# Optimization experiments

Measured on AMD Instinct MI355X. Metric: run time of the kernel, lower is better.

The kernel has to match this reference:

```python
import jax, jax.numpy as jnp
from jax import lax
import numpy as np

NUM_HEAD = 12
EPS = 1e-5            # torch LayerNorm default
NEG_INF = 1.0e12      # self.inf_value in the source
LEAKY_SLOPE = 0.01    # torch LeakyReLU default
MASK_FIRST = True     # maskedAtten=True applies only to block 0


def _layer_norm(x, s, b):
    m = jnp.mean(x, axis=-1, keepdims=True)
    v = jnp.var(x, axis=-1, keepdims=True)
    return (x - m) / jnp.sqrt(v + EPS) * s + b


def _forward(x, conv_w, conv_b, pos, ln0_s, ln0_b, Wq, bq, Wk, bk, Wv, bv,
             Wo, bo, ln1_s, ln1_b, W1, b1, W2, b2, proj_w, proj_b):
    B, C, H, W = x.shape
    E = conv_w.shape[0]
    P = conv_w.shape[-1]
    hd = E // NUM_HEAD

    # patch embed: Conv2d(C, E, P, stride=P)
    h = lax.conv_general_dilated(x, conv_w, (P, P), 'VALID',
                                 dimension_numbers=('NCHW', 'OIHW', 'NCHW'))
    h = h + conv_b[None, :, None, None]
    L = h.shape[2] * h.shape[3]
    h = h.reshape(B, E, L).transpose(0, 2, 1) + pos  # (B, L, E)

    causal = jnp.triu(jnp.ones((L, L), dtype=bool), 1)
    n_layers = Wq.shape[0]
    for i in range(n_layers):
        # --- attention block ---
        xn = _layer_norm(h, ln0_s[i], ln0_b[i])
        q = (xn @ Wq[i] + bq[i]).reshape(B, L, NUM_HEAD, hd).transpose(0, 2, 1, 3)
        k = (xn @ Wk[i] + bk[i]).reshape(B, L, NUM_HEAD, hd).transpose(0, 2, 1, 3)
        v = (xn @ Wv[i] + bv[i]).reshape(B, L, NUM_HEAD, hd).transpose(0, 2, 1, 3)
        scores = jnp.einsum('bhqd,bhkd->bhqk', q, k) * (hd ** -0.5)
        if i == 0 and MASK_FIRST:
            scores = jnp.where(causal, -NEG_INF, scores)
        a = jax.nn.softmax(scores, axis=-1)
        o = jnp.einsum('bhqk,bhkd->bhqd', a, v)  # (B, NH, L, hd)
        # faithful to torch source: reshape(bs, l, emb) WITHOUT permuting heads back
        o = o.reshape(B, L, E)
        o = o @ Wo[i] + bo[i]
        h = o + h  # residual onto pre-LN input
        # --- MLP block ---
        xr = _layer_norm(h, ln1_s[i], ln1_b[i])
        m = xr @ W1[i] + b1[i]
        m = jnp.where(m >= 0, m, LEAKY_SLOPE * m)
        m = m @ W2[i] + b2[i]
        h = m + xr  # residual onto post-LN (as in source)

    y = h @ proj_w + proj_b               # (B, L, C*P*P)
    y = y.transpose(0, 2, 1).reshape(B, C, H, W)
    return y


def setup_inputs() -> dict:
    key = jax.random.key(0)
    B, C, H, W = 8, 3, 384, 384
    P, E, NL = 16, 768, 8
    FF = 4 * E
    L = (H // P) * (W // P)  # 576
    CPP = C * P * P          # 768
    s = 0.02
    ks = jax.random.split(key, 24)
    f32 = jnp.float32
    inp = {
        'x': jax.random.normal(ks[0], (B, C, H, W), f32),
        'conv_w': jax.random.normal(ks[1], (E, C, P, P), f32) * s,
        'conv_b': jax.random.normal(ks[2], (E,), f32) * s,
        'pos': jax.random.normal(ks[3], (1, L, E), f32),
        'ln0_s': jnp.ones((NL, E), f32),
        'ln0_b': jnp.zeros((NL, E), f32),
        'Wq': jax.random.normal(ks[4], (NL, E, E), f32) * s,
        'bq': jax.random.normal(ks[5], (NL, E), f32) * s,
        'Wk': jax.random.normal(ks[6], (NL, E, E), f32) * s,
        'bk': jax.random.normal(ks[7], (NL, E), f32) * s,
        'Wv': jax.random.normal(ks[8], (NL, E, E), f32) * s,
        'bv': jax.random.normal(ks[9], (NL, E), f32) * s,
        'Wo': jax.random.normal(ks[10], (NL, E, E), f32) * s,
        'bo': jax.random.normal(ks[11], (NL, E), f32) * s,
        'ln1_s': jnp.ones((NL, E), f32),
        'ln1_b': jnp.zeros((NL, E), f32),
        'W1': jax.random.normal(ks[12], (NL, E, FF), f32) * s,
        'b1': jax.random.normal(ks[13], (NL, FF), f32) * s,
        'W2': jax.random.normal(ks[14], (NL, FF, E), f32) * s,
        'b2': jax.random.normal(ks[15], (NL, E), f32) * s,
        'proj_w': jax.random.normal(ks[16], (E, CPP), f32) * s,
        'proj_b': jax.random.normal(ks[17], (CPP,), f32) * s,
    }
    return inp


def reference(x, conv_w, conv_b, pos, ln0_s, ln0_b, Wq, bq, Wk, bk, Wv, bv,
              Wo, bo, ln1_s, ln1_b, W1, b1, W2, b2, proj_w, proj_b):
    return _forward(x, conv_w, conv_b, pos, ln0_s, ln0_b, Wq, bq, Wk, bk,
                    Wv, bv, Wo, bo, ln1_s, ln1_b, W1, b1, W2, b2,
                    proj_w, proj_b)
```

## Files before the change

kernel.cpp:

```cpp
#include <hip/hip_runtime.h>
#include <hip/hip_bf16.h>
#include <stdint.h>

#define NLAYERS 8
#define LSEQ 576
#define EMB 768
#define NHEAD 12
#define HDIM 64
#define FFDIM 3072
#define BLROWS 4608

typedef __attribute__((ext_vector_type(8))) short short8;
typedef __attribute__((ext_vector_type(4))) float floatx4;

__device__ __forceinline__ float b2f(short s) {
    union { float f; uint32_t u; } x; x.u = ((uint32_t)(uint16_t)s) << 16; return x.f;
}
__device__ __forceinline__ short f2b(float f) {
    union { float f; uint32_t u; } x; x.f = f;
    uint32_t r = x.u + 0x7fffu + ((x.u >> 16) & 1u);
    return (short)(r >> 16);
}

#define GLDS16(gp, lp) __builtin_amdgcn_global_load_lds( \
    (const __attribute__((address_space(1))) void*)(gp), \
    (__attribute__((address_space(3))) void*)(lp), 16, 0, 0)

__device__ __forceinline__ void xcd_remap(int& bx, int& by) {
    const int gx = gridDim.x;
    const int n  = gx * gridDim.y;
    const int orig = by * gx + bx;
    const int q = n >> 3, r = n & 7;
    const int xcd = orig & 7;
    const int wgid = (xcd < r ? xcd * (q + 1) : r * (q + 1) + (xcd - r) * q) + (orig >> 3);
    bx = wgid % gx;
    by = wgid / gx;
}

template<bool ADD_POS, bool RES_F32, bool LEAKY, bool OUT_F32>
__global__ __launch_bounds__(256)
void gemm_bt(const short* __restrict__ A, const short* __restrict__ Bt,
             const float* __restrict__ bias, const float* __restrict__ pos,
             const float* __restrict__ resf, void* __restrict__ Cout,
             int N, int K)
{
    __shared__ short As[2 * 64 * 64];
    __shared__ short Bs[2 * 128 * 64];
    int bx = blockIdx.x, by = blockIdx.y;
    xcd_remap(bx, by);
    const int t    = threadIdx.x;
    const int lane = t & 63;
    const int w    = t >> 6;
    const int m0   = by * 64;
    const int n0   = bx * 128;
    const int wm   = (w >> 1) * 32;
    const int wn   = (w & 1) * 64;

    floatx4 acc[2][4];
#pragma unroll
    for (int i = 0; i < 2; ++i)
#pragma unroll
        for (int j = 0; j < 4; ++j)
            acc[i][j] = (floatx4){0.f, 0.f, 0.f, 0.f};

    const int srow = t >> 3;
    const int sch  = t & 7;

    const short* Ag = A  + (size_t)m0 * K;
    const short* Bg = Bt + (size_t)n0 * K;

#define STAGE(buf, k0)                                                              \
    {                                                                               \
        _Pragma("unroll")                                                           \
        for (int i = 0; i < 2; ++i) {                                               \
            int row = srow + i * 32;                                                \
            GLDS16(Ag + (size_t)row * K + (k0) + ((sch ^ (row & 7)) << 3),          \
                   &As[(buf) * 4096 + (size_t)(t + i * 256) * 8]);                  \
        }                                                                           \
        _Pragma("unroll")                                                           \
        for (int i = 0; i < 4; ++i) {                                               \
            int row = srow + i * 32;                                                \
            GLDS16(Bg + (size_t)row * K + (k0) + ((sch ^ (row & 7)) << 3),          \
                   &Bs[(buf) * 8192 + (size_t)(t + i * 256) * 8]);                  \
        }                                                                           \
    }

    STAGE(0, 0);
    __syncthreads();
    int cur = 0;
    for (int k0 = 0; k0 < K; k0 += 64) {
        if (k0 + 64 < K) STAGE(cur ^ 1, k0 + 64);
#pragma unroll
        for (int ks = 0; ks < 2; ++ks) {
            short8 af[2], bf[4];
#pragma unroll
            for (int i = 0; i < 2; ++i) {
                int row = wm + i * 16 + (lane & 15);
                int ch  = (ks * 4 + (lane >> 4)) ^ (row & 7);
                af[i] = *(const short8*)&As[cur * 4096 + row * 64 + ch * 8];
            }
#pragma unroll
            for (int j = 0; j < 4; ++j) {
                int row = wn + j * 16 + (lane & 15);
                int ch  = (ks * 4 + (lane >> 4)) ^ (row & 7);
                bf[j] = *(const short8*)&Bs[cur * 8192 + row * 64 + ch * 8];
            }
#pragma unroll
            for (int i = 0; i < 2; ++i)
#pragma unroll
                for (int j = 0; j < 4; ++j)
                    acc[i][j] = __builtin_amdgcn_mfma_f32_16x16x32_bf16(af[i], bf[j], acc[i][j], 0, 0, 0);
        }
        __syncthreads();
        cur ^= 1;
    }
#undef STAGE

    const int colb = n0 + wn + (lane & 15);
    const int rowb = m0 + wm + ((lane >> 4) * 4);
#pragma unroll
    for (int i = 0; i < 2; ++i) {
#pragma unroll
        for (int j = 0; j < 4; ++j) {
            const int col = colb + j * 16;
            const float bv = bias[col];
#pragma unroll
            for (int r = 0; r < 4; ++r) {
                const int row = rowb + i * 16 + r;
                float v = acc[i][j][r] + bv;
                if constexpr (ADD_POS) v += pos[(size_t)(row % LSEQ) * N + col];
                if constexpr (RES_F32) v += resf[(size_t)row * N + col];
                if constexpr (LEAKY)   v = v >= 0.f ? v : 0.01f * v;
                if constexpr (OUT_F32) ((float*)Cout)[(size_t)row * N + col] = v;
                else                   ((short*)Cout)[(size_t)row * N + col] = f2b(v);
            }
        }
    }
}

__global__ __launch_bounds__(256)
void ln_kernel(const float* __restrict__ h, const float* __restrict__ g,
               const float* __restrict__ bbias, short* __restrict__ outb,
               float* __restrict__ outf)
{
    const int row = blockIdx.x;
    const float* x = h + (size_t)row * EMB;
    const int t = threadIdx.x;
    float v0 = x[t], v1 = x[t + 256], v2 = x[t + 512];
    float s  = v0 + v1 + v2;
    float ss = v0 * v0 + v1 * v1 + v2 * v2;
#pragma unroll
    for (int m = 1; m < 64; m <<= 1) {
        s  += __shfl_xor(s, m, 64);
        ss += __shfl_xor(ss, m, 64);
    }
    __shared__ float red[8];
    if ((t & 63) == 0) { red[t >> 6] = s; red[4 + (t >> 6)] = ss; }
    __syncthreads();
    float S  = red[0] + red[1] + red[2] + red[3];
    float SS = red[4] + red[5] + red[6] + red[7];
    float mean = S * (1.f / 768.f);
    float var  = SS * (1.f / 768.f) - mean * mean;
    float rstd = rsqrtf(var + 1e-5f);
    const size_t base = (size_t)row * EMB;
#pragma unroll
    for (int q = 0; q < 3; ++q) {
        int e = t + q * 256;
        float v = (q == 0 ? v0 : (q == 1 ? v1 : v2));
        float y = (v - mean) * rstd * g[e] + bbias[e];
        outb[base + e] = f2b(y);
        if (outf) outf[base + e] = y;
    }
}

__global__ __launch_bounds__(256)
void repack_kv(const short* __restrict__ qkv, short* __restrict__ kp, short* __restrict__ vt)
{
    const int kt = blockIdx.x, bh = blockIdx.y;
    const int b = bh / 12, h = bh % 12;
    const int t = threadIdx.x;
#pragma unroll
    for (int i = 0; i < 2; ++i) {
        int flat = i * 256 + t;
        int key = flat >> 3, c = flat & 7;
        short8 vK = *(const short8*)(qkv + ((size_t)(b * LSEQ) + kt * 64 + key) * 2304 + 768 + h * 64 + c * 8);
        *(short8*)(kp + ((size_t)bh * LSEQ + kt * 64 + key) * 64 + 8 * (c ^ (key & 7))) = vK;
    }
    __shared__ short tile[64][65];
    const int tx = t & 63, ty = t >> 6;
#pragma unroll
    for (int r = 0; r < 16; ++r) {
        int k = ty * 16 + r;
        tile[k][tx] = qkv[((size_t)(b * LSEQ) + kt * 64 + k) * 2304 + 1536 + h * 64 + tx];
    }
    __syncthreads();
#pragma unroll
    for (int r = 0; r < 16; ++r) {
        int d = ty * 16 + r;
        vt[((size_t)bh * 64 + d) * LSEQ + kt * 64 + (tx ^ ((d & 7) << 3))] = tile[tx][d];
    }
}

__global__ __launch_bounds__(256)
void attn_mfma(const short* __restrict__ qkv, const short* __restrict__ kp,
               const short* __restrict__ vt, short* __restrict__ oout, int causal)
{
    const int qt = blockIdx.x, bh = blockIdx.y;
    const int b = bh / 12, h = bh % 12;
    const int t = threadIdx.x, lane = t & 63, w = t >> 6;

    __shared__ short Ks[64 * 64];
    __shared__ short Vs[64 * 64];
    __shared__ short Plds[4][16][72];

    const int nrow = lane & 15;
    const int kch  = (lane >> 4) * 8;
    const int swz  = (lane & 7) << 3;

    short8 aq[2];
    {
        const short* qrow = qkv + ((size_t)(b * LSEQ) + qt * 64 + w * 16 + nrow) * 2304 + h * 64 + kch;
        aq[0] = *(const short8*)qrow;
        aq[1] = *(const short8*)(qrow + 32);
    }

    float m[4], lsum[4];
    floatx4 oacc[4];
#pragma unroll
    for (int r = 0; r < 4; ++r) { m[r] = -3e38f; lsum[r] = 0.f; }
#pragma unroll
    for (int j = 0; j < 4; ++j) oacc[j] = (floatx4){0.f, 0.f, 0.f, 0.f};

    const int ktend = causal ? qt : 8;
    const short* ksrc = kp + ((size_t)bh * LSEQ) * 64;
    const short* vsrc = vt + ((size_t)bh * 64) * LSEQ;

    for (int kt = 0; kt <= ktend; ++kt) {
        __syncthreads();
        {
            const short* kt_src = ksrc + (size_t)(kt * 64) * 64;
            GLDS16(kt_src + (size_t)t * 8,          &Ks[(size_t)t * 8]);
            GLDS16(kt_src + (size_t)(t + 256) * 8,  &Ks[(size_t)(t + 256) * 8]);
            int f0 = t, f1 = t + 256;
            GLDS16(vsrc + (size_t)(f0 >> 3) * LSEQ + kt * 64 + (f0 & 7) * 8, &Vs[(size_t)f0 * 8]);
            GLDS16(vsrc + (size_t)(f1 >> 3) * LSEQ + kt * 64 + (f1 & 7) * 8, &Vs[(size_t)f1 * 8]);
        }
        __syncthreads();

        floatx4 sc[4];
#pragma unroll
        for (int j = 0; j < 4; ++j) sc[j] = (floatx4){0.f, 0.f, 0.f, 0.f};
#pragma unroll
        for (int s = 0; s < 2; ++s) {
#pragma unroll
            for (int j = 0; j < 4; ++j) {
                short8 bk = *(const short8*)&Ks[(16 * j + nrow) * 64 + ((kch + 32 * s) ^ swz)];
                sc[j] = __builtin_amdgcn_mfma_f32_16x16x32_bf16(aq[s], bk, sc[j], 0, 0, 0);
            }
        }
        float sv[4][4];
#pragma unroll
        for (int j = 0; j < 4; ++j)
#pragma unroll
            for (int r = 0; r < 4; ++r) {
                float v = sc[j][r] * 0.125f;
                if (causal && kt == qt) {
                    int key = kt * 64 + 16 * j + nrow;
                    int qr  = qt * 64 + w * 16 + (lane >> 4) * 4 + r;
                    if (key > qr) v = -1e12f;
                }
                sv[j][r] = v;
            }
#pragma unroll
        for (int r = 0; r < 4; ++r) {
            float tm = fmaxf(fmaxf(sv[0][r], sv[1][r]), fmaxf(sv[2][r], sv[3][r]));
            tm = fmaxf(tm, __shfl_xor(tm, 1, 64));
            tm = fmaxf(tm, __shfl_xor(tm, 2, 64));
            tm = fmaxf(tm, __shfl_xor(tm, 4, 64));
            tm = fmaxf(tm, __shfl_xor(tm, 8, 64));
            float nm = fmaxf(m[r], tm);
            float c  = __expf(m[r] - nm);
            m[r] = nm;
            float ps = 0.f;
#pragma unroll
            for (int j = 0; j < 4; ++j) {
                float p = __expf(sv[j][r] - nm);
                sv[j][r] = p;
                ps += p;
            }
            lsum[r] = lsum[r] * c + ps;
#pragma unroll
            for (int j = 0; j < 4; ++j) oacc[j][r] *= c;
        }
#pragma unroll
        for (int j = 0; j < 4; ++j)
#pragma unroll
            for (int r = 0; r < 4; ++r)
                Plds[w][(lane >> 4) * 4 + r][16 * j + nrow] = f2b(sv[j][r]);
        short8 ap[2];
#pragma unroll
        for (int s = 0; s < 2; ++s)
            ap[s] = *(const short8*)&Plds[w][nrow][kch + 32 * s];
#pragma unroll
        for (int s = 0; s < 2; ++s) {
#pragma unroll
            for (int j = 0; j < 4; ++j) {
                short8 bv = *(const short8*)&Vs[(16 * j + nrow) * 64 + ((kch + 32 * s) ^ swz)];
                oacc[j] = __builtin_amdgcn_mfma_f32_16x16x32_bf16(ap[s], bv, oacc[j], 0, 0, 0);
            }
        }
    }

    float inv[4];
#pragma unroll
    for (int r = 0; r < 4; ++r) {
        float L = lsum[r];
        L += __shfl_xor(L, 1, 64);
        L += __shfl_xor(L, 2, 64);
        L += __shfl_xor(L, 4, 64);
        L += __shfl_xor(L, 8, 64);
        inv[r] = 1.f / L;
    }
#pragma unroll
    for (int j = 0; j < 4; ++j)
#pragma unroll
        for (int r = 0; r < 4; ++r) {
            size_t lq = (size_t)qt * 64 + w * 16 + (lane >> 4) * 4 + r;
            oout[((size_t)bh * LSEQ + lq) * 64 + 16 * j + nrow] = f2b(oacc[j][r] * inv[r]);
        }
}

__global__ void transpose_f2b(const float* __restrict__ in, short* __restrict__ out,
                              int R, int C, long long ibs, long long obs)
{
    __shared__ float tile[32][33];
    const int b = blockIdx.z;
    const float* inb = in + (long long)b * ibs;
    short* outb = out + (long long)b * obs;
    const int r0 = blockIdx.y * 32, c0 = blockIdx.x * 32;
    const int tx = threadIdx.x, ty = threadIdx.y;
#pragma unroll
    for (int i = 0; i < 32; i += 8) tile[ty + i][tx] = inb[(size_t)(r0 + ty + i) * C + c0 + tx];
    __syncthreads();
#pragma unroll
    for (int i = 0; i < 32; i += 8) outb[(size_t)(c0 + ty + i) * R + r0 + tx] = f2b(tile[tx][ty + i]);
}

__global__ void transpose_f2f(const float* __restrict__ in, float* __restrict__ out,
                              int R, int C, long long ibs, long long obs)
{
    __shared__ float tile[32][33];
    const int b = blockIdx.z;
    const float* inb = in + (long long)b * ibs;
    float* outb = out + (long long)b * obs;
    const int r0 = blockIdx.y * 32, c0 = blockIdx.x * 32;
    const int tx = threadIdx.x, ty = threadIdx.y;
#pragma unroll
    for (int i = 0; i < 32; i += 8) tile[ty + i][tx] = inb[(size_t)(r0 + ty + i) * C + c0 + tx];
    __syncthreads();
#pragma unroll
    for (int i = 0; i < 32; i += 8) outb[(size_t)(c0 + ty + i) * R + r0 + tx] = tile[tx][ty + i];
}

__global__ void concat_qkv_bias(const float* __restrict__ bq, const float* __restrict__ bk,
                                const float* __restrict__ bv, float* __restrict__ out)
{
    int i = blockIdx.x * 256 + threadIdx.x;
    int layer = i / 2304, j = i % 2304;
    float v;
    if (j < 768)       v = bq[layer * 768 + j];
    else if (j < 1536) v = bk[layer * 768 + j - 768];
    else               v = bv[layer * 768 + j - 1536];
    out[i] = v;
}

__global__ void im2col_kernel(const float* __restrict__ x, short* __restrict__ xcol)
{
    const size_t idx = (size_t)blockIdx.x * 256 + threadIdx.x;
    const int k = (int)(idx % 768);
    const size_t m = idx / 768;
    const int c  = k >> 8;
    const int ky = (k >> 4) & 15;
    const int kx = k & 15;
    const int b  = (int)(m / 576);
    const int l  = (int)(m % 576);
    const int ph = l / 24, pw = l % 24;
    xcol[idx] = f2b(x[((size_t)(b * 3 + c) * 384 + ph * 16 + ky) * 384 + pw * 16 + kx]);
}

__global__ void cast_f32_b16(const float* __restrict__ in, short* __restrict__ out, int n)
{
    int i = blockIdx.x * 256 + threadIdx.x;
    if (i < n) out[i] = f2b(in[i]);
}

extern "C" void kernel_launch(void* const* d_in, const int* in_sizes, int n_in,
                              void* d_out, int out_size, void* d_ws, size_t ws_size,
                              hipStream_t stream)
{
    const float* x      = (const float*)d_in[0];
    const float* conv_w = (const float*)d_in[1];
    const float* conv_b = (const float*)d_in[2];
    const float* pos    = (const float*)d_in[3];
    const float* ln0_s  = (const float*)d_in[4];
    const float* ln0_b  = (const float*)d_in[5];
    const float* Wq     = (const float*)d_in[6];
    const float* bq     = (const float*)d_in[7];
    const float* Wk     = (const float*)d_in[8];
    const float* bk     = (const float*)d_in[9];
    const float* Wv     = (const float*)d_in[10];
    const float* bv     = (const float*)d_in[11];
    const float* Wo     = (const float*)d_in[12];
    const float* bo     = (const float*)d_in[13];
    const float* ln1_s  = (const float*)d_in[14];
    const float* ln1_b  = (const float*)d_in[15];
    const float* W1     = (const float*)d_in[16];
    const float* b1     = (const float*)d_in[17];
    const float* W2     = (const float*)d_in[18];
    const float* b2     = (const float*)d_in[19];
    const float* proj_w = (const float*)d_in[20];
    const float* proj_b = (const float*)d_in[21];

    char* ws = (char*)d_ws;
    short* qkvT  = (short*)(ws);
    short* woT   = (short*)(ws + 28311552);
    short* w1T   = (short*)(ws + 37748736);
    short* w2T   = (short*)(ws + 75497472);
    short* projT = (short*)(ws + 113246208);
    float* qkvb  = (float*)(ws + 114425856);
    short* tmpA  = (short*)(ws + 114499584);
    float* h     = (float*)(ws + 142811136);
    short* xn    = (short*)(ws + 156966912);
    short* xrb   = (short*)(ws + 164044800);
    float* xrf   = (float*)(ws + 171122688);
    short* qkv   = (short*)(ws + 185278464);
    short* o     = (short*)(ws + 206512128);
    short* convB = (short*)(ws + 213590016);

    short* kp = tmpA;
    short* vt = tmpA + 3538944;

    dim3 tb(32, 8);
    transpose_f2b<<<dim3(24, 24, 8), tb, 0, stream>>>(Wq, qkvT,           768, 768, 589824, 1769472);
    transpose_f2b<<<dim3(24, 24, 8), tb, 0, stream>>>(Wk, qkvT + 589824,  768, 768, 589824, 1769472);
    transpose_f2b<<<dim3(24, 24, 8), tb, 0, stream>>>(Wv, qkvT + 1179648, 768, 768, 589824, 1769472);
    transpose_f2b<<<dim3(24, 24, 8), tb, 0, stream>>>(Wo, woT,            768, 768, 589824, 589824);
    transpose_f2b<<<dim3(96, 24, 8), tb, 0, stream>>>(W1, w1T,            768, 3072, 2359296, 2359296);
    transpose_f2b<<<dim3(24, 96, 8), tb, 0, stream>>>(W2, w2T,            3072, 768, 2359296, 2359296);
    transpose_f2b<<<dim3(24, 24, 1), tb, 0, stream>>>(proj_w, projT,      768, 768, 0, 0);
    cast_f32_b16<<<2304, 256, 0, stream>>>(conv_w, convB, 589824);
    concat_qkv_bias<<<72, 256, 0, stream>>>(bq, bk, bv, qkvb);

    im2col_kernel<<<13824, 256, 0, stream>>>(x, tmpA);
    gemm_bt<true, false, false, true><<<dim3(6, 72), 256, 0, stream>>>(
        tmpA, convB, conv_b, pos, nullptr, h, 768, 768);

    for (int i = 0; i < NLAYERS; ++i) {
        ln_kernel<<<4608, 256, 0, stream>>>(h, ln0_s + i * 768, ln0_b + i * 768, xn, nullptr);
        gemm_bt<false, false, false, false><<<dim3(18, 72), 256, 0, stream>>>(
            xn, qkvT + (size_t)i * 1769472, qkvb + i * 2304, nullptr, nullptr, qkv, 2304, 768);
        repack_kv<<<dim3(9, 96), 256, 0, stream>>>(qkv, kp, vt);
        attn_mfma<<<dim3(9, 96), 256, 0, stream>>>(qkv, kp, vt, o, i == 0 ? 1 : 0);
        gemm_bt<false, true, false, true><<<dim3(6, 72), 256, 0, stream>>>(
            o, woT + (size_t)i * 589824, bo + i * 768, nullptr, h, h, 768, 768);
        ln_kernel<<<4608, 256, 0, stream>>>(h, ln1_s + i * 768, ln1_b + i * 768, xrb, xrf);
        gemm_bt<false, false, true, false><<<dim3(24, 72), 256, 0, stream>>>(
            xrb, w1T + (size_t)i * 2359296, b1 + i * 3072, nullptr, nullptr, tmpA, 3072, 768);
        gemm_bt<false, true, false, true><<<dim3(6, 72), 256, 0, stream>>>(
            tmpA, w2T + (size_t)i * 2359296, b2 + i * 768, nullptr, xrf, h, 768, 3072);
    }

    short* hb = xn;
    float* yf = (float*)tmpA;
    cast_f32_b16<<<13824, 256, 0, stream>>>(h, hb, 4608 * 768);
    gemm_bt<false, false, false, true><<<dim3(6, 72), 256, 0, stream>>>(
        hb, projT, proj_b, nullptr, nullptr, yf, 768, 768);
    transpose_f2f<<<dim3(24, 18, 8), tb, 0, stream>>>(yf, (float*)d_out, 576, 768, 442368, 442368);
}
```

Measured before the change: 1.695 ms.

## Add triple-buffered LDS pipeline for N=768 GEMMs and read bf16 residual

Adds a DEPTH template parameter to the GEMM so the N=768 GEMMs (small grids of 432 blocks) use a three-stage LDS ring with explicit vmcnt waits and a single barrier per k-step. This keeps more global loads in flight to hide memory latency when occupancy is low. Separately, the W2 GEMM now reads the post-LN residual as bf16 instead of a separate f32 copy, which drops the f32 write in the LN kernel and halves the residual read. The bf16 residual loses precision in the skip connection, and the hand-written waitcnt counts must match the number of loads issued per stage.

```diff
diff --git a/kernel.cpp b/kernel.cpp
--- a/kernel.cpp
+++ b/kernel.cpp
@@ -37,15 +37,15 @@
     by = wgid / gx;
 }
 
-template<bool ADD_POS, bool RES_F32, bool LEAKY, bool OUT_F32>
+template<int DEPTH, int RES, bool ADD_POS, bool LEAKY, bool OUT_F32>
 __global__ __launch_bounds__(256)
 void gemm_bt(const short* __restrict__ A, const short* __restrict__ Bt,
              const float* __restrict__ bias, const float* __restrict__ pos,
-             const float* __restrict__ resf, void* __restrict__ Cout,
+             const void* __restrict__ res, void* __restrict__ Cout,
              int N, int K)
 {
-    __shared__ short As[2 * 64 * 64];
-    __shared__ short Bs[2 * 128 * 64];
+    __shared__ short As[DEPTH * 64 * 64];
+    __shared__ short Bs[DEPTH * 128 * 64];
     int bx = blockIdx.x, by = blockIdx.y;
     xcd_remap(bx, by);
     const int t    = threadIdx.x;
@@ -65,9 +65,9 @@
 
     const int srow = t >> 3;
     const int sch  = t & 7;
-
     const short* Ag = A  + (size_t)m0 * K;
     const short* Bg = Bt + (size_t)n0 * K;
+    const int nt = K >> 6;
 
 #define STAGE(buf, k0)                                                              \
     {                                                                               \
@@ -85,36 +85,65 @@
         }                                                                           \
     }
 
-    STAGE(0, 0);
-    __syncthreads();
-    int cur = 0;
-    for (int k0 = 0; k0 < K; k0 += 64) {
-        if (k0 + 64 < K) STAGE(cur ^ 1, k0 + 64);
-#pragma unroll
-        for (int ks = 0; ks < 2; ++ks) {
-            short8 af[2], bf[4];
-#pragma unroll
-            for (int i = 0; i < 2; ++i) {
-                int row = wm + i * 16 + (lane & 15);
-                int ch  = (ks * 4 + (lane >> 4)) ^ (row & 7);
-                af[i] = *(const short8*)&As[cur * 4096 + row * 64 + ch * 8];
+#define COMPUTE(buf)                                                                \
+    {                                                                               \
+        _Pragma("unroll")                                                           \
+        for (int ks = 0; ks < 2; ++ks) {                                            \
+            short8 af[2], bf[4];                                                    \
+            _Pragma("unroll")                                                       \
+            for (int i = 0; i < 2; ++i) {                                           \
+                int row = wm + i * 16 + (lane & 15);                                \
+                int ch  = (ks * 4 + (lane >> 4)) ^ (row & 7);                       \
+                af[i] = *(const short8*)&As[(buf) * 4096 + row * 64 + ch * 8];      \
+            }                                                                       \
+            _Pragma("unroll")                                                       \
+            for (int j = 0; j < 4; ++j) {                                           \
+                int row = wn + j * 16 + (lane & 15);                                \
+                int ch  = (ks * 4 + (lane >> 4)) ^ (row & 7);                       \
+                bf[j] = *(const short8*)&Bs[(buf) * 8192 + row * 64 + ch * 8];      \
+            }                                                                       \
+            _Pragma("unroll")                                                       \
+            for (int i = 0; i < 2; ++i)                                             \
+                _Pragma("unroll")                                                   \
+                for (int j = 0; j < 4; ++j)                                         \
+                    acc[i][j] = __builtin_amdgcn_mfma_f32_16x16x32_bf16(            \
+                        af[i], bf[j], acc[i][j], 0, 0, 0);                          \
+        }                                                                           \
+    }
+
+    if constexpr (DEPTH == 2) {
+        STAGE(0, 0);
+        __syncthreads();
+        int cur = 0;
+        for (int k0 = 0; k0 < K; k0 += 64) {
+            if (k0 + 64 < K) STAGE(cur ^ 1, k0 + 64);
+            COMPUTE(cur);
+            __syncthreads();
+            cur ^= 1;
+        }
+    } else {
+        STAGE(0, 0);
+        STAGE(1, 64);
+        asm volatile("s_waitcnt vmcnt(6)" ::: "memory");
+        __builtin_amdgcn_sched_barrier(0);
+        __builtin_amdgcn_s_barrier();
+        int cur = 0, stg = 2;
+        for (int tt = 0; tt < nt; ++tt) {
+            if (tt + 2 < nt) STAGE(stg, (tt + 2) << 6);
+            COMPUTE(cur);
+            if (tt + 1 < nt) {
+                if (tt + 2 < nt) { asm volatile("s_waitcnt vmcnt(6)" ::: "memory"); }
+                else             { asm volatile("s_waitcnt vmcnt(0)" ::: "memory"); }
+                __builtin_amdgcn_sched_barrier(0);
+                __builtin_amdgcn_s_barrier();
+                __builtin_amdgcn_sched_barrier(0);
             }
-#pragma unroll
-            for (int j = 0; j < 4; ++j) {
-                int row = wn + j * 16 + (lane & 15);
-                int ch  = (ks * 4 + (lane >> 4)) ^ (row & 7);
-                bf[j] = *(const short8*)&Bs[cur * 8192 + row * 64 + ch * 8];
-            }
-#pragma unroll
-            for (int i = 0; i < 2; ++i)
-#pragma unroll
-                for (int j = 0; j < 4; ++j)
-                    acc[i][j] = __builtin_amdgcn_mfma_f32_16x16x32_bf16(af[i], bf[j], acc[i][j], 0, 0, 0);
-        }
-        __syncthreads();
-        cur ^= 1;
+            cur = (cur + 1 == DEPTH) ? 0 : cur + 1;
+            stg = (stg + 1 == DEPTH) ? 0 : stg + 1;
+        }
     }
 #undef STAGE
+#undef COMPUTE
 
     const int colb = n0 + wn + (lane & 15);
     const int rowb = m0 + wm + ((lane >> 4) * 4);
@@ -129,7 +158,8 @@
                 const int row = rowb + i * 16 + r;
                 float v = acc[i][j][r] + bv;
                 if constexpr (ADD_POS) v += pos[(size_t)(row % LSEQ) * N + col];
-                if constexpr (RES_F32) v += resf[(size_t)row * N + col];
+                if constexpr (RES == 1) v += ((const float*)res)[(size_t)row * N + col];
+                if constexpr (RES == 2) v += b2f(((const short*)res)[(size_t)row * N + col]);
                 if constexpr (LEAKY)   v = v >= 0.f ? v : 0.01f * v;
                 if constexpr (OUT_F32) ((float*)Cout)[(size_t)row * N + col] = v;
                 else                   ((short*)Cout)[(size_t)row * N + col] = f2b(v);
@@ -432,7 +462,6 @@
     float* h     = (float*)(ws + 142811136);
     short* xn    = (short*)(ws + 156966912);
     short* xrb   = (short*)(ws + 164044800);
-    float* xrf   = (float*)(ws + 171122688);
     short* qkv   = (short*)(ws + 185278464);
     short* o     = (short*)(ws + 206512128);
     short* convB = (short*)(ws + 213590016);
@@ -452,28 +481,28 @@
     concat_qkv_bias<<<72, 256, 0, stream>>>(bq, bk, bv, qkvb);
 
     im2col_kernel<<<13824, 256, 0, stream>>>(x, tmpA);
-    gemm_bt<true, false, false, true><<<dim3(6, 72), 256, 0, stream>>>(
+    gemm_bt<3, 0, true, false, true><<<dim3(6, 72), 256, 0, stream>>>(
         tmpA, convB, conv_b, pos, nullptr, h, 768, 768);
 
     for (int i = 0; i < NLAYERS; ++i) {
         ln_kernel<<<4608, 256, 0, stream>>>(h, ln0_s + i * 768, ln0_b + i * 768, xn, nullptr);
-        gemm_bt<false, false, false, false><<<dim3(18, 72), 256, 0, stream>>>(
+        gemm_bt<2, 0, false, false, false><<<dim3(18, 72), 256, 0, stream>>>(
             xn, qkvT + (size_t)i * 1769472, qkvb + i * 2304, nullptr, nullptr, qkv, 2304, 768);
         repack_kv<<<dim3(9, 96), 256, 0, stream>>>(qkv, kp, vt);
         attn_mfma<<<dim3(9, 96), 256, 0, stream>>>(qkv, kp, vt, o, i == 0 ? 1 : 0);
-        gemm_bt<false, true, false, true><<<dim3(6, 72), 256, 0, stream>>>(
+        gemm_bt<3, 1, false, false, true><<<dim3(6, 72), 256, 0, stream>>>(
             o, woT + (size_t)i * 589824, bo + i * 768, nullptr, h, h, 768, 768);
-        ln_kernel<<<4608, 256, 0, stream>>>(h, ln1_s + i * 768, ln1_b + i * 768, xrb, xrf);
-        gemm_bt<false, false, true, false><<<dim3(24, 72), 256, 0, stream>>>(
+        ln_kernel<<<4608, 256, 0, stream>>>(h, ln1_s + i * 768, ln1_b + i * 768, xrb, nullptr);
+        gemm_bt<2, 0, false, true, false><<<dim3(24, 72), 256, 0, stream>>>(
             xrb, w1T + (size_t)i * 2359296, b1 + i * 3072, nullptr, nullptr, tmpA, 3072, 768);
-        gemm_bt<false, true, false, true><<<dim3(6, 72), 256, 0, stream>>>(
-            tmpA, w2T + (size_t)i * 2359296, b2 + i * 768, nullptr, xrf, h, 768, 3072);
+        gemm_bt<3, 2, false, false, true><<<dim3(6, 72), 256, 0, stream>>>(
+            tmpA, w2T + (size_t)i * 2359296, b2 + i * 768, nullptr, xrb, h, 768, 3072);
     }
 
     short* hb = xn;
     float* yf = (float*)tmpA;
     cast_f32_b16<<<13824, 256, 0, stream>>>(h, hb, 4608 * 768);
-    gemm_bt<false, false, false, true><<<dim3(6, 72), 256, 0, stream>>>(
+    gemm_bt<3, 0, false, false, true><<<dim3(6, 72), 256, 0, stream>>>(
         hb, projT, proj_b, nullptr, nullptr, yf, 768, 768);
     transpose_f2f<<<dim3(24, 18, 8), tb, 0, stream>>>(yf, (float*)d_out, 576, 768, 442368, 442368);
 }
```

Result: faster. 1.640 ms (-3.2%).

## Enlarge GEMM tile to 128x128 and fuse K/V repack into QKV epilogue

Applied to the files above, without the earlier changes.

The GEMM block tile grows from 64x128 to 128x128, with each wave computing 64x64, so the B operand is reused across more rows per LDS load. The QKV GEMM epilogue now scatters Q to a compact buffer and K/V straight into the swizzled per-head layouts, which removes the separate repack_kv kernel and its round trip through global memory. The MLP residual is read from the bf16 LN output instead of a separate f32 copy, so that buffer is no longer written. In exchange, grids have half as many blocks, register and LDS use per block rise, the K/V epilogue stores are scattered 2-byte writes, and the residual loses precision by being rounded to bf16.

```diff
diff --git a/kernel.cpp b/kernel.cpp
--- a/kernel.cpp
+++ b/kernel.cpp
@@ -37,45 +37,45 @@
     by = wgid / gx;
 }
 
-template<bool ADD_POS, bool RES_F32, bool LEAKY, bool OUT_F32>
+template<int RES, bool ADD_POS, bool LEAKY, bool OUT_F32, bool QKV>
 __global__ __launch_bounds__(256)
 void gemm_bt(const short* __restrict__ A, const short* __restrict__ Bt,
              const float* __restrict__ bias, const float* __restrict__ pos,
-             const float* __restrict__ resf, void* __restrict__ Cout,
+             const void* __restrict__ res, void* __restrict__ Cout,
+             short* __restrict__ kp, short* __restrict__ vt,
              int N, int K)
 {
-    __shared__ short As[2 * 64 * 64];
+    __shared__ short As[2 * 128 * 64];
     __shared__ short Bs[2 * 128 * 64];
     int bx = blockIdx.x, by = blockIdx.y;
     xcd_remap(bx, by);
     const int t    = threadIdx.x;
     const int lane = t & 63;
     const int w    = t >> 6;
-    const int m0   = by * 64;
+    const int m0   = by * 128;
     const int n0   = bx * 128;
-    const int wm   = (w >> 1) * 32;
+    const int wm   = (w >> 1) * 64;
     const int wn   = (w & 1) * 64;
 
-    floatx4 acc[2][4];
-#pragma unroll
-    for (int i = 0; i < 2; ++i)
+    floatx4 acc[4][4];
+#pragma unroll
+    for (int i = 0; i < 4; ++i)
 #pragma unroll
         for (int j = 0; j < 4; ++j)
             acc[i][j] = (floatx4){0.f, 0.f, 0.f, 0.f};
 
     const int srow = t >> 3;
     const int sch  = t & 7;
-
     const short* Ag = A  + (size_t)m0 * K;
     const short* Bg = Bt + (size_t)n0 * K;
 
 #define STAGE(buf, k0)                                                              \
     {                                                                               \
         _Pragma("unroll")                                                           \
-        for (int i = 0; i < 2; ++i) {                                               \
+        for (int i = 0; i < 4; ++i) {                                               \
             int row = srow + i * 32;                                                \
             GLDS16(Ag + (size_t)row * K + (k0) + ((sch ^ (row & 7)) << 3),          \
-                   &As[(buf) * 4096 + (size_t)(t + i * 256) * 8]);                  \
+                   &As[(buf) * 8192 + (size_t)(t + i * 256) * 8]);                  \
         }                                                                           \
         _Pragma("unroll")                                                           \
         for (int i = 0; i < 4; ++i) {                                               \
@@ -92,12 +92,12 @@
         if (k0 + 64 < K) STAGE(cur ^ 1, k0 + 64);
 #pragma unroll
         for (int ks = 0; ks < 2; ++ks) {
-            short8 af[2], bf[4];
-#pragma unroll
-            for (int i = 0; i < 2; ++i) {
+            short8 af[4], bf[4];
+#pragma unroll
+            for (int i = 0; i < 4; ++i) {
                 int row = wm + i * 16 + (lane & 15);
                 int ch  = (ks * 4 + (lane >> 4)) ^ (row & 7);
-                af[i] = *(const short8*)&As[cur * 4096 + row * 64 + ch * 8];
+                af[i] = *(const short8*)&As[cur * 8192 + row * 64 + ch * 8];
             }
 #pragma unroll
             for (int j = 0; j < 4; ++j) {
@@ -106,7 +106,7 @@
                 bf[j] = *(const short8*)&Bs[cur * 8192 + row * 64 + ch * 8];
             }
 #pragma unroll
-            for (int i = 0; i < 2; ++i)
+            for (int i = 0; i < 4; ++i)
 #pragma unroll
                 for (int j = 0; j < 4; ++j)
                     acc[i][j] = __builtin_amdgcn_mfma_f32_16x16x32_bf16(af[i], bf[j], acc[i][j], 0, 0, 0);
@@ -119,7 +119,7 @@
     const int colb = n0 + wn + (lane & 15);
     const int rowb = m0 + wm + ((lane >> 4) * 4);
 #pragma unroll
-    for (int i = 0; i < 2; ++i) {
+    for (int i = 0; i < 4; ++i) {
 #pragma unroll
         for (int j = 0; j < 4; ++j) {
             const int col = colb + j * 16;
@@ -129,10 +129,28 @@
                 const int row = rowb + i * 16 + r;
                 float v = acc[i][j][r] + bv;
                 if constexpr (ADD_POS) v += pos[(size_t)(row % LSEQ) * N + col];
-                if constexpr (RES_F32) v += resf[(size_t)row * N + col];
+                if constexpr (RES == 1) v += ((const float*)res)[(size_t)row * N + col];
+                if constexpr (RES == 2) v += b2f(((const short*)res)[(size_t)row * N + col]);
                 if constexpr (LEAKY)   v = v >= 0.f ? v : 0.01f * v;
-                if constexpr (OUT_F32) ((float*)Cout)[(size_t)row * N + col] = v;
-                else                   ((short*)Cout)[(size_t)row * N + col] = f2b(v);
+                if constexpr (QKV) {
+                    const int b = row / LSEQ, l = row % LSEQ;
+                    const short sv16 = f2b(v);
+                    if (col < 768) {
+                        ((short*)Cout)[(size_t)row * 768 + col] = sv16;
+                    } else if (col < 1536) {
+                        const int d = col - 768, hh = d >> 6, dd = d & 63;
+                        const size_t bh = (size_t)b * 12 + hh;
+                        kp[(bh * LSEQ + l) * 64 + (dd & 7) + (((dd >> 3) ^ (l & 7)) << 3)] = sv16;
+                    } else {
+                        const int d = col - 1536, hh = d >> 6, dd = d & 63;
+                        const size_t bh = (size_t)b * 12 + hh;
+                        vt[(bh * 64 + dd) * LSEQ + (l & ~63) + ((l & 63) ^ ((dd & 7) << 3))] = sv16;
+                    }
+                } else if constexpr (OUT_F32) {
+                    ((float*)Cout)[(size_t)row * N + col] = v;
+                } else {
+                    ((short*)Cout)[(size_t)row * N + col] = f2b(v);
+                }
             }
         }
     }
@@ -174,35 +192,7 @@
 }
 
 __global__ __launch_bounds__(256)
-void repack_kv(const short* __restrict__ qkv, short* __restrict__ kp, short* __restrict__ vt)
-{
-    const int kt = blockIdx.x, bh = blockIdx.y;
-    const int b = bh / 12, h = bh % 12;
-    const int t = threadIdx.x;
-#pragma unroll
-    for (int i = 0; i < 2; ++i) {
-        int flat = i * 256 + t;
-        int key = flat >> 3, c = flat & 7;
-        short8 vK = *(const short8*)(qkv + ((size_t)(b * LSEQ) + kt * 64 + key) * 2304 + 768 + h * 64 + c * 8);
-        *(short8*)(kp + ((size_t)bh * LSEQ + kt * 64 + key) * 64 + 8 * (c ^ (key & 7))) = vK;
-    }
-    __shared__ short tile[64][65];
-    const int tx = t & 63, ty = t >> 6;
-#pragma unroll
-    for (int r = 0; r < 16; ++r) {
-        int k = ty * 16 + r;
-        tile[k][tx] = qkv[((size_t)(b * LSEQ) + kt * 64 + k) * 2304 + 1536 + h * 64 + tx];
-    }
-    __syncthreads();
-#pragma unroll
-    for (int r = 0; r < 16; ++r) {
-        int d = ty * 16 + r;
-        vt[((size_t)bh * 64 + d) * LSEQ + kt * 64 + (tx ^ ((d & 7) << 3))] = tile[tx][d];
-    }
-}
-
-__global__ __launch_bounds__(256)
-void attn_mfma(const short* __restrict__ qkv, const short* __restrict__ kp,
+void attn_mfma(const short* __restrict__ qbuf, const short* __restrict__ kp,
                const short* __restrict__ vt, short* __restrict__ oout, int causal)
 {
     const int qt = blockIdx.x, bh = blockIdx.y;
@@ -219,7 +209,7 @@
 
     short8 aq[2];
     {
-        const short* qrow = qkv + ((size_t)(b * LSEQ) + qt * 64 + w * 16 + nrow) * 2304 + h * 64 + kch;
+        const short* qrow = qbuf + ((size_t)(b * LSEQ) + qt * 64 + w * 16 + nrow) * 768 + h * 64 + kch;
         aq[0] = *(const short8*)qrow;
         aq[1] = *(const short8*)(qrow + 32);
     }
@@ -432,8 +422,7 @@
     float* h     = (float*)(ws + 142811136);
     short* xn    = (short*)(ws + 156966912);
     short* xrb   = (short*)(ws + 164044800);
-    float* xrf   = (float*)(ws + 171122688);
-    short* qkv   = (short*)(ws + 185278464);
+    short* qbuf  = (short*)(ws + 185278464);
     short* o     = (short*)(ws + 206512128);
     short* convB = (short*)(ws + 213590016);
 
@@ -452,28 +441,27 @@
     concat_qkv_bias<<<72, 256, 0, stream>>>(bq, bk, bv, qkvb);
 
     im2col_kernel<<<13824, 256, 0, stream>>>(x, tmpA);
-    gemm_bt<true, false, false, true><<<dim3(6, 72), 256, 0, stream>>>(
-        tmpA, convB, conv_b, pos, nullptr, h, 768, 768);
+    gemm_bt<0, true, false, true, false><<<dim3(6, 36), 256, 0, stream>>>(
+        tmpA, convB, conv_b, pos, nullptr, h, nullptr, nullptr, 768, 768);
 
     for (int i = 0; i < NLAYERS; ++i) {
         ln_kernel<<<4608, 256, 0, stream>>>(h, ln0_s + i * 768, ln0_b + i * 768, xn, nullptr);
-        gemm_bt<false, false, false, false><<<dim3(18, 72), 256, 0, stream>>>(
-            xn, qkvT + (size_t)i * 1769472, qkvb + i * 2304, nullptr, nullptr, qkv, 2304, 768);
-        repack_kv<<<dim3(9, 96), 256, 0, stream>>>(qkv, kp, vt);
-        attn_mfma<<<dim3(9, 96), 256, 0, stream>>>(qkv, kp, vt, o, i == 0 ? 1 : 0);
-        gemm_bt<false, true, false, true><<<dim3(6, 72), 256, 0, stream>>>(
-            o, woT + (size_t)i * 589824, bo + i * 768, nullptr, h, h, 768, 768);
-        ln_kernel<<<4608, 256, 0, stream>>>(h, ln1_s + i * 768, ln1_b + i * 768, xrb, xrf);
-        gemm_bt<false, false, true, false><<<dim3(24, 72), 256, 0, stream>>>(
-            xrb, w1T + (size_t)i * 2359296, b1 + i * 3072, nullptr, nullptr, tmpA, 3072, 768);
-        gemm_bt<false, true, false, true><<<dim3(6, 72), 256, 0, stream>>>(
-            tmpA, w2T + (size_t)i * 2359296, b2 + i * 768, nullptr, xrf, h, 768, 3072);
+        gemm_bt<0, false, false, false, true><<<dim3(18, 36), 256, 0, stream>>>(
+            xn, qkvT + (size_t)i * 1769472, qkvb + i * 2304, nullptr, nullptr, qbuf, kp, vt, 2304, 768);
+        attn_mfma<<<dim3(9, 96), 256, 0, stream>>>(qbuf, kp, vt, o, i == 0 ? 1 : 0);
+        gemm_bt<1, false, false, true, false><<<dim3(6, 36), 256, 0, stream>>>(
+            o, woT + (size_t)i * 589824, bo + i * 768, nullptr, h, h, nullptr, nullptr, 768, 768);
+        ln_kernel<<<4608, 256, 0, stream>>>(h, ln1_s + i * 768, ln1_b + i * 768, xrb, nullptr);
+        gemm_bt<0, false, true, false, false><<<dim3(24, 36), 256, 0, stream>>>(
+            xrb, w1T + (size_t)i * 2359296, b1 + i * 3072, nullptr, nullptr, tmpA, nullptr, nullptr, 3072, 768);
+        gemm_bt<2, false, false, true, false><<<dim3(6, 36), 256, 0, stream>>>(
+            tmpA, w2T + (size_t)i * 2359296, b2 + i * 768, nullptr, xrb, h, nullptr, nullptr, 768, 3072);
     }
 
     short* hb = xn;
     float* yf = (float*)tmpA;
     cast_f32_b16<<<13824, 256, 0, stream>>>(h, hb, 4608 * 768);
-    gemm_bt<false, false, false, true><<<dim3(6, 72), 256, 0, stream>>>(
-        hb, projT, proj_b, nullptr, nullptr, yf, 768, 768);
+    gemm_bt<0, false, false, true, false><<<dim3(6, 36), 256, 0, stream>>>(
+        hb, projT, proj_b, nullptr, nullptr, yf, nullptr, nullptr, 768, 768);
     transpose_f2f<<<dim3(24, 18, 8), tb, 0, stream>>>(yf, (float*)d_out, 576, 768, 442368, 442368);
 }
```

Result: no change. 1.699 ms (+0.2%).
